# Kernel tuning notes

Hardware: AMD Instinct MI355X
Metric: run time of the kernel (lower is better)

## Reference

```python
import jax, jax.numpy as jnp
import numpy as np

B, C, H, W = 32, 256, 96, 96
K = 3
PAD = K // 2


def setup_inputs() -> dict:
    key = jax.random.key(0)
    k1, k2, k3 = jax.random.split(key, 3)
    x = jax.random.normal(k1, (B, C, H, W), dtype=jnp.float32)
    # 1x1 conv params collapsed to dense matrices (act on pooled (B,C) vectors)
    w1 = jax.random.normal(k2, (C, C), dtype=jnp.float32) * 0.02
    b1 = jnp.zeros((C,), dtype=jnp.float32)
    w2 = jax.random.normal(k3, (C * K * K, C), dtype=jnp.float32) * 0.02
    b2 = jnp.zeros((C * K * K,), dtype=jnp.float32)
    return {"x": x, "w1": w1, "b1": b1, "w2": w2, "b2": b2}


def reference(x, w1, b1, w2, b2):
    Bs, Cs, Hs, Ws = x.shape
    # dynamic_net: global avg pool -> 1x1 conv -> GELU (exact) -> 1x1 conv
    pooled = x.mean(axis=(2, 3))                       # (B, C)
    h = jax.nn.gelu(pooled @ w1.T + b1, approximate=False)
    wdyn = (h @ w2.T + b2).reshape(Bs, Cs, K * K)      # (B, C, k^2)

    # reflect pad, then fused per-sample/per-channel 3x3 weighted sum
    xp = jnp.pad(x, ((0, 0), (0, 0), (PAD, PAD), (PAD, PAD)), mode="reflect")
    out = jnp.zeros_like(x)
    for i in range(K):
        for j in range(K):
            idx = i * K + j  # matches F.unfold row-major kernel ordering
            out = out + xp[:, :, i:i + Hs, j:j + Ws] * wdyn[:, :, idx, None, None]
    return out
```

## Files before the change

### kernel.cpp

```cpp
#include <hip/hip_runtime.h>
#include <math.h>

#define Bq 32
#define Cq 256
#define Hq 96
#define Wq 96
#define HWq (Hq * Wq)
#define KKq 9
#define CKq (Cq * KKq)
#define NPLANES (Bq * Cq)

__global__ __launch_bounds__(256) void pool_kernel(const float* __restrict__ x,
                                                   float* __restrict__ pooled) {
    int plane = blockIdx.x;
    const float4* px = (const float4*)(x + (size_t)plane * HWq);
    int t = threadIdx.x;
    float s = 0.f;
#pragma unroll
    for (int i = 0; i < 9; ++i) {
        float4 v = px[t + i * 256];
        s += v.x + v.y + v.z + v.w;
    }
    for (int off = 32; off > 0; off >>= 1) s += __shfl_down(s, off, 64);
    __shared__ float wsum[4];
    if ((t & 63) == 0) wsum[t >> 6] = s;
    __syncthreads();
    if (t == 0) {
        pooled[plane] = (wsum[0] + wsum[1] + wsum[2] + wsum[3]) * (1.0f / HWq);
    }
}

__global__ __launch_bounds__(256) void fc1_kernel(const float* __restrict__ pooled,
                                                  const float* __restrict__ w1,
                                                  const float* __restrict__ b1,
                                                  float* __restrict__ h) {
    int b = blockIdx.x;
    int j = threadIdx.x;
    __shared__ float p[Cq];
    p[j] = pooled[b * Cq + j];
    __syncthreads();
    const float4* wrow = (const float4*)(w1 + (size_t)j * Cq);
    float acc = b1[j];
#pragma unroll 4
    for (int k = 0; k < Cq / 4; ++k) {
        float4 w = wrow[k];
        acc += p[4 * k] * w.x + p[4 * k + 1] * w.y + p[4 * k + 2] * w.z + p[4 * k + 3] * w.w;
    }
    float g = 0.5f * acc * (1.0f + erff(acc * 0.70710678118654752440f));
    h[b * Cq + j] = g;
}

__global__ __launch_bounds__(256) void fc2_kernel(const float* __restrict__ hbuf,
                                                  const float* __restrict__ w2,
                                                  const float* __restrict__ b2,
                                                  float* __restrict__ wdyn) {
    int b = blockIdx.y;
    int m = blockIdx.x * 256 + threadIdx.x;
    __shared__ float hs[Cq];
    hs[threadIdx.x] = hbuf[b * Cq + threadIdx.x];
    __syncthreads();
    const float4* wrow = (const float4*)(w2 + (size_t)m * Cq);
    float acc = b2[m];
#pragma unroll 4
    for (int k = 0; k < Cq / 4; ++k) {
        float4 w = wrow[k];
        acc += hs[4 * k] * w.x + hs[4 * k + 1] * w.y + hs[4 * k + 2] * w.z + hs[4 * k + 3] * w.w;
    }
    wdyn[b * CKq + m] = acc;
}

__global__ __launch_bounds__(256) void conv_kernel(const float* __restrict__ x,
                                                   const float* __restrict__ wdyn,
                                                   float* __restrict__ out) {
    int plane = (NPLANES - 1) - blockIdx.x;
    const float* xp = x + (size_t)plane * HWq;
    float* op = out + (size_t)plane * HWq;
    const float* wd = wdyn + (size_t)plane * KKq;
    float w0 = wd[0], w1 = wd[1], w2 = wd[2];
    float w3 = wd[3], w4 = wd[4], w5 = wd[5];
    float w6 = wd[6], w7 = wd[7], w8 = wd[8];
    int t = threadIdx.x;
    int gbase = t + blockIdx.y * 768;
#pragma unroll
    for (int it = 0; it < 3; ++it) {
        int g = gbase + it * 256;
        int hh = g / 24;
        int wq = (g % 24) * 4;
        int rm = (hh == 0) ? 1 : hh - 1;
        int rp = (hh == 95) ? 94 : hh + 1;
        const float* r0 = xp + rm * Wq;
        const float* r1 = xp + hh * Wq;
        const float* r2 = xp + rp * Wq;
        int li = (wq == 0) ? 1 : wq - 1;
        int ri = (wq == 92) ? 94 : wq + 4;
        float4 c0 = *(const float4*)(r0 + wq);
        float4 c1 = *(const float4*)(r1 + wq);
        float4 c2 = *(const float4*)(r2 + wq);
        float l0 = r0[li], l1 = r1[li], l2 = r2[li];
        float q0 = r0[ri], q1 = r1[ri], q2 = r2[ri];
        float4 o;
        o.x = w0 * l0    + w1 * c0.x + w2 * c0.y;
        o.y = w0 * c0.x  + w1 * c0.y + w2 * c0.z;
        o.z = w0 * c0.y  + w1 * c0.z + w2 * c0.w;
        o.w = w0 * c0.z  + w1 * c0.w + w2 * q0;
        o.x += w3 * l1   + w4 * c1.x + w5 * c1.y;
        o.y += w3 * c1.x + w4 * c1.y + w5 * c1.z;
        o.z += w3 * c1.y + w4 * c1.z + w5 * c1.w;
        o.w += w3 * c1.z + w4 * c1.w + w5 * q1;
        o.x += w6 * l2   + w7 * c2.x + w8 * c2.y;
        o.y += w6 * c2.x + w7 * c2.y + w8 * c2.z;
        o.z += w6 * c2.y + w7 * c2.z + w8 * c2.w;
        o.w += w6 * c2.z + w7 * c2.w + w8 * q2;
        *(float4*)(op + (size_t)g * 4) = o;
    }
}

extern "C" void kernel_launch(void* const* d_in, const int* in_sizes, int n_in,
                              void* d_out, int out_size, void* d_ws, size_t ws_size,
                              hipStream_t stream) {
    const float* x  = (const float*)d_in[0];
    const float* w1 = (const float*)d_in[1];
    const float* b1 = (const float*)d_in[2];
    const float* w2 = (const float*)d_in[3];
    const float* b2 = (const float*)d_in[4];
    float* out = (float*)d_out;

    float* pooled = (float*)d_ws;
    float* h      = pooled + Bq * Cq;
    float* wdyn   = h + Bq * Cq;

    pool_kernel<<<NPLANES, 256, 0, stream>>>(x, pooled);
    fc1_kernel<<<Bq, 256, 0, stream>>>(pooled, w1, b1, h);
    fc2_kernel<<<dim3(CKq / 256, Bq), 256, 0, stream>>>(h, w2, b2, wdyn);
    conv_kernel<<<dim3(NPLANES, 3), 256, 0, stream>>>(x, wdyn, out);
}
```

Measured before the change: 633.9 us.

## Fuse fc1 into fc2, one conv block per plane, nontemporal output stores

New measurement: 615.1 us. 3.0% less time.

```diff
diff --git a/kernel.cpp b/kernel.cpp
--- a/kernel.cpp
+++ b/kernel.cpp
@@ -9,6 +9,8 @@
 #define KKq 9
 #define CKq (Cq * KKq)
 #define NPLANES (Bq * Cq)
+
+typedef float f4 __attribute__((ext_vector_type(4)));
 
 __global__ __launch_bounds__(256) void pool_kernel(const float* __restrict__ x,
                                                    float* __restrict__ pooled) {
@@ -30,13 +32,16 @@
     }
 }
 
-__global__ __launch_bounds__(256) void fc1_kernel(const float* __restrict__ pooled,
-                                                  const float* __restrict__ w1,
-                                                  const float* __restrict__ b1,
-                                                  float* __restrict__ h) {
-    int b = blockIdx.x;
+__global__ __launch_bounds__(256) void fc_fused(const float* __restrict__ pooled,
+                                                const float* __restrict__ w1,
+                                                const float* __restrict__ b1,
+                                                const float* __restrict__ w2,
+                                                const float* __restrict__ b2,
+                                                float* __restrict__ wdyn) {
+    int b = blockIdx.y;
     int j = threadIdx.x;
     __shared__ float p[Cq];
+    __shared__ float hs[Cq];
     p[j] = pooled[b * Cq + j];
     __syncthreads();
     const float4* wrow = (const float4*)(w1 + (size_t)j * Cq);
@@ -46,27 +51,17 @@
         float4 w = wrow[k];
         acc += p[4 * k] * w.x + p[4 * k + 1] * w.y + p[4 * k + 2] * w.z + p[4 * k + 3] * w.w;
     }
-    float g = 0.5f * acc * (1.0f + erff(acc * 0.70710678118654752440f));
-    h[b * Cq + j] = g;
-}
-
-__global__ __launch_bounds__(256) void fc2_kernel(const float* __restrict__ hbuf,
-                                                  const float* __restrict__ w2,
-                                                  const float* __restrict__ b2,
-                                                  float* __restrict__ wdyn) {
-    int b = blockIdx.y;
-    int m = blockIdx.x * 256 + threadIdx.x;
-    __shared__ float hs[Cq];
-    hs[threadIdx.x] = hbuf[b * Cq + threadIdx.x];
+    hs[j] = 0.5f * acc * (1.0f + erff(acc * 0.70710678118654752440f));
     __syncthreads();
-    const float4* wrow = (const float4*)(w2 + (size_t)m * Cq);
-    float acc = b2[m];
+    int m = blockIdx.x * 256 + j;
+    const float4* w2row = (const float4*)(w2 + (size_t)m * Cq);
+    float a2 = b2[m];
 #pragma unroll 4
     for (int k = 0; k < Cq / 4; ++k) {
-        float4 w = wrow[k];
-        acc += hs[4 * k] * w.x + hs[4 * k + 1] * w.y + hs[4 * k + 2] * w.z + hs[4 * k + 3] * w.w;
+        float4 w = w2row[k];
+        a2 += hs[4 * k] * w.x + hs[4 * k + 1] * w.y + hs[4 * k + 2] * w.z + hs[4 * k + 3] * w.w;
     }
-    wdyn[b * CKq + m] = acc;
+    wdyn[b * CKq + m] = a2;
 }
 
 __global__ __launch_bounds__(256) void conv_kernel(const float* __restrict__ x,
@@ -80,10 +75,9 @@
     float w3 = wd[3], w4 = wd[4], w5 = wd[5];
     float w6 = wd[6], w7 = wd[7], w8 = wd[8];
     int t = threadIdx.x;
-    int gbase = t + blockIdx.y * 768;
 #pragma unroll
-    for (int it = 0; it < 3; ++it) {
-        int g = gbase + it * 256;
+    for (int it = 0; it < 9; ++it) {
+        int g = t + it * 256;
         int hh = g / 24;
         int wq = (g % 24) * 4;
         int rm = (hh == 0) ? 1 : hh - 1;
@@ -111,7 +105,7 @@
         o.y += w6 * c2.x + w7 * c2.y + w8 * c2.z;
         o.z += w6 * c2.y + w7 * c2.z + w8 * c2.w;
         o.w += w6 * c2.z + w7 * c2.w + w8 * q2;
-        *(float4*)(op + (size_t)g * 4) = o;
+        __builtin_nontemporal_store(*(f4*)&o, (f4*)(op + (size_t)g * 4));
     }
 }
 
@@ -126,11 +120,9 @@
     float* out = (float*)d_out;
 
     float* pooled = (float*)d_ws;
-    float* h      = pooled + Bq * Cq;
-    float* wdyn   = h + Bq * Cq;
+    float* wdyn   = pooled + Bq * Cq;
 
     pool_kernel<<<NPLANES, 256, 0, stream>>>(x, pooled);
-    fc1_kernel<<<Bq, 256, 0, stream>>>(pooled, w1, b1, h);
-    fc2_kernel<<<dim3(CKq / 256, Bq), 256, 0, stream>>>(h, w2, b2, wdyn);
-    conv_kernel<<<dim3(NPLANES, 3), 256, 0, stream>>>(x, wdyn, out);
+    fc_fused<<<dim3(CKq / 256, Bq), 256, 0, stream>>>(pooled, w1, b1, w2, b2, wdyn);
+    conv_kernel<<<NPLANES, 256, 0, stream>>>(x, wdyn, out);
 }
```
